# Kernel optimization log

Hardware: AMD Instinct MI355X
Metric: run time of the kernel (lower is better)

Reference implementation:

```python
import jax, jax.numpy as jnp
import numpy as np

T = 36  # num_frames


def box_cxcywh_to_xyxy(b):
    cx, cy, w, h = jnp.split(b, 4, axis=-1)
    return jnp.concatenate([cx - 0.5 * w, cy - 0.5 * h, cx + 0.5 * w, cy + 0.5 * h], axis=-1)


def multi_iou(b1, b2):
    # b1: [Q,1,T,4], b2: [1,N,T,4], xyxy -> iou [Q,N,T]
    lt = jnp.maximum(b1[..., :2], b2[..., :2])
    rb = jnp.minimum(b1[..., 2:], b2[..., 2:])
    wh = jnp.clip(rb - lt, 0.0)
    inter = wh[..., 0] * wh[..., 1]
    a1 = (b1[..., 2] - b1[..., 0]) * (b1[..., 3] - b1[..., 1])
    a2 = (b2[..., 2] - b2[..., 0]) * (b2[..., 3] - b2[..., 1])
    union = a1 + a2 - inter
    return inter / union


def setup_inputs() -> dict:
    key = jax.random.key(0)
    k1, k2, k3, k4, k5, k6 = jax.random.split(key, 6)
    Q, N, C = 2048, 128, 42
    return {
        "pred_logits": jax.random.normal(k1, (T * Q, C), dtype=jnp.float32),
        "pred_boxes": jax.random.uniform(k2, (T * Q, 4), dtype=jnp.float32),
        "tgt_labels": jax.random.randint(k3, (N * T,), 0, C - 1),
        "tgt_boxes": jax.random.uniform(k4, (N * T, 4), dtype=jnp.float32),
        "tgt_valid": jax.random.randint(k5, (N * T,), 0, 2, dtype=jnp.int32),
        "tgt_original_valid": jax.random.randint(k6, (N * T,), 0, 2, dtype=jnp.int32),
    }


def reference(pred_logits, pred_boxes, tgt_labels, tgt_boxes, tgt_valid, tgt_original_valid):
    # Cost-matrix computation of SoftMaxHungarianMatcher (cost_class=cost_bbox=cost_giou=1,
    # use_giou=False, use_l1_distance_sum=False). The scipy linear_sum_assignment step is
    # CPU-serial / non-tensor and excluded; output is the [Q,N] cost fed to it.
    C = pred_logits.shape[-1]
    Q = pred_logits.shape[0] // T
    N = tgt_labels.shape[0] // T
    num_classes = C - 1  # background index

    probs = jax.nn.softmax(pred_logits, axis=-1).reshape(T, Q, C).transpose(1, 0, 2)  # [Q,T,C]
    boxes = pred_boxes.reshape(T, Q, 4).transpose(1, 0, 2)                            # [Q,T,4]
    tboxes = tgt_boxes.reshape(N, T, 4)
    valid = tgt_valid.reshape(N, T).astype(probs.dtype)                               # [N,T]
    ovalid = tgt_original_valid.reshape(N, T)
    ids = jnp.where(ovalid == 0, num_classes, tgt_labels.reshape(N, T))               # [N,T]

    denom = valid.sum(-1)  # [N] (per-instance count of valid frames)

    # class cost: -mean_t p(q, t, ids[n,t]) over valid frames
    gathered = probs[:, jnp.arange(T)[None, :], ids]                                  # [Q,N,T]
    class_cost = -(gathered * valid).sum(-1) / denom                                  # [Q,N]

    # bbox L1 cost: mean over (valid frames, 4 coords)
    l1 = jnp.abs(boxes[:, None] - tboxes[None]).mean(-1)                              # [Q,N,T]
    bbox_cost = (l1 * valid).sum(-1) / denom                                          # [Q,N]

    # IoU cost: -mean_t iou over valid frames
    iou = multi_iou(box_cxcywh_to_xyxy(boxes)[:, None], box_cxcywh_to_xyxy(tboxes)[None])
    iou_cost = -(iou * valid).sum(-1) / denom                                         # [Q,N]

    return class_cost + bbox_cost + iou_cost
```

## Files before the change

kernel.cpp:

```cpp
#include <hip/hip_runtime.h>
#include <hip/hip_bf16.h>


constexpr int T = 36;
constexpr int Q = 2048;
constexpr int C = 42;
constexpr int N = 128;

__global__ __launch_bounds__(256) void softmax_transpose_kernel(
    const float* __restrict__ logits, __hip_bfloat16* __restrict__ P2) {
  constexpr int QB = 64;
  constexpr int LS = C + 1;

  __shared__ float tile[QB * LS];
  __shared__ float s_max[4 * QB];
  __shared__ float s_sum[4 * QB];
  __shared__ float s_rinv[QB];

  const int t = blockIdx.y;
  const int q0 = blockIdx.x * QB;
  const int tid = threadIdx.x;

  const float* src = logits + ((size_t)t * Q + q0) * C;
  for (int i = tid; i < QB * C; i += 256) {
    int r = i / C, c = i % C;
    tile[r * LS + c] = src[i];
  }
  __syncthreads();

  const int part = tid >> 6;
  const int row = tid & 63;
  const int c0 = (part < 2) ? part * 11 : 22 + (part - 2) * 10;
  const int c1 = (part < 2) ? c0 + 11 : c0 + 10;

  float m = -1e30f;
  for (int c = c0; c < c1; ++c) m = fmaxf(m, tile[row * LS + c]);
  s_max[part * QB + row] = m;
  __syncthreads();

  m = fmaxf(fmaxf(s_max[row], s_max[QB + row]),
            fmaxf(s_max[2 * QB + row], s_max[3 * QB + row]));
  float s = 0.f;
  for (int c = c0; c < c1; ++c) {
    float e = __expf(tile[row * LS + c] - m);
    tile[row * LS + c] = e;
    s += e;
  }
  s_sum[part * QB + row] = s;
  __syncthreads();

  if (part == 0) {
    float stot = s_sum[row] + s_sum[QB + row] + s_sum[2 * QB + row] +
                 s_sum[3 * QB + row];
    s_rinv[row] = 1.f / stot;
  }
  __syncthreads();

  for (int i = tid; i < QB * C / 2; i += 256) {
    int c = i >> 5;
    int r2 = i & 31;
    float v0 = tile[(2 * r2) * LS + c] * s_rinv[2 * r2];
    float v1 = tile[(2 * r2 + 1) * LS + c] * s_rinv[2 * r2 + 1];
    __hip_bfloat162 pk;
    pk.x = __float2bfloat16(v0);
    pk.y = __float2bfloat16(v1);
    *(__hip_bfloat162*)(P2 + (size_t)(t * C + c) * Q + q0 + 2 * r2) = pk;
  }
}

constexpr int NB = 8;

__global__ __launch_bounds__(512) void cost_kernel(
    const __hip_bfloat16* __restrict__ P2, const float* __restrict__ pred_boxes,
    const int* __restrict__ labels, const float* __restrict__ tboxes,
    const int* __restrict__ valid, const int* __restrict__ ovalid,
    float* __restrict__ out) {
  constexpr int RS = NB + 1;

  const int q0 = blockIdx.x * 64;
  const int n0 = blockIdx.y * NB;
  const int tid = threadIdx.x;
  const int lane = tid & 63;
  const int wave = tid >> 6;
  const int q = q0 + lane;

  __shared__ float4 s_tbA[NB * T];
  __shared__ float4 s_tbB[NB * T];
  __shared__ int s_pk[NB * T];
  __shared__ float s_rden[NB];
  __shared__ float s_red[8 * 64 * RS];

  for (int i = tid; i < NB * T; i += 512) {
    int n = n0 + i / T;
    int t = i % T;
    int g = n * T + t;
    int id = (ovalid[g] == 0) ? (C - 1) : labels[g];
    s_pk[i] = (valid[g] << 24) | (id * (Q * 2));
    float4 tb = ((const float4*)tboxes)[g];
    s_tbA[i] = tb;
    float4 B;
    B.x = fmaf(-0.5f, tb.z, tb.x);
    B.y = fmaf(-0.5f, tb.w, tb.y);
    B.z = fmaf(0.5f, tb.z, tb.x);
    B.w = fmaf(0.5f, tb.w, tb.y);
    s_tbB[i] = B;
  }
  if (tid < NB) {
    int n = n0 + tid;
    int s = 0;
    for (int t = 0; t < T; ++t) s += valid[n * T + t];
    s_rden[tid] = 1.f / (float)s;
  }
  __syncthreads();

  float acc[NB];
#pragma unroll
  for (int j = 0; j < NB; ++j) acc[j] = 0.f;

  const int t_begin = (wave * T) / 8;
  const int t_end = ((wave + 1) * T) / 8;

  for (int t = t_begin; t < t_end; ++t) {
    float4 pb = ((const float4*)pred_boxes)[t * Q + q];
    float px1 = fmaf(-0.5f, pb.z, pb.x);
    float py1 = fmaf(-0.5f, pb.w, pb.y);
    float px2 = fmaf(0.5f, pb.z, pb.x);
    float py2 = fmaf(0.5f, pb.w, pb.y);
    float area_p = pb.z * pb.w;
    const char* pcol = (const char*)(P2 + (size_t)t * C * Q + q);

#pragma unroll
    for (int j = 0; j < NB; ++j) {
      int pk = s_pk[j * T + t];
      if (pk & (1 << 24)) {
        float4 tb = s_tbA[j * T + t];
        float4 xy = s_tbB[j * T + t];
        float p = __bfloat162float(
            *(const __hip_bfloat16*)(pcol + (pk & 0xFFFFFF)));

        float s = fabsf(pb.x - tb.x) + fabsf(pb.y - tb.y) +
                  fabsf(pb.z - tb.z) + fabsf(pb.w - tb.w);
        float iw = fmaxf(fminf(px2, xy.z) - fmaxf(px1, xy.x), 0.f);
        float ih = fmaxf(fminf(py2, xy.w) - fmaxf(py1, xy.y), 0.f);
        float inter = iw * ih;
        float uni = fmaf(tb.z, tb.w, area_p) - inter;
        float r = __builtin_amdgcn_rcpf(uni);
        acc[j] = fmaf(0.25f, s, acc[j]) - p - inter * r;
      }
    }
  }

#pragma unroll
  for (int j = 0; j < NB; ++j) s_red[(wave * 64 + lane) * RS + j] = acc[j];
  __syncthreads();

  {
    int ql = tid >> 3;
    int j = tid & 7;
    float s = 0.f;
#pragma unroll
    for (int w = 0; w < 8; ++w) s += s_red[(w * 64 + ql) * RS + j];
    out[(size_t)(q0 + ql) * N + n0 + j] = s * s_rden[j];
  }
}

extern "C" void kernel_launch(void* const* d_in, const int* in_sizes, int n_in,
                              void* d_out, int out_size, void* d_ws, size_t ws_size,
                              hipStream_t stream) {
  const float* logits = (const float*)d_in[0];
  const float* pboxes = (const float*)d_in[1];
  const int* labels = (const int*)d_in[2];
  const float* tboxes = (const float*)d_in[3];
  const int* valid = (const int*)d_in[4];
  const int* ovalid = (const int*)d_in[5];
  float* out = (float*)d_out;

  __hip_bfloat16* P2 = (__hip_bfloat16*)d_ws;

  dim3 g1(Q / 64, T);
  softmax_transpose_kernel<<<g1, 256, 0, stream>>>(logits, P2);

  dim3 g2(Q / 64, N / NB);
  cost_kernel<<<g2, 512, 0, stream>>>(P2, pboxes, labels, tboxes, valid, ovalid, out);
}
```

Before: 86.27 us.

## Vectorize softmax without max-shift and repartition cost kernel per target

The softmax kernel now loads logits as float4, applies exp directly without subtracting the row max, and reduces row sums with wave shuffles instead of shared-memory staging. The cost kernel changes from 8 waves splitting frames with 8 targets per thread to 4 targets per block, each wave pair handling one target over half the frames. It also writes the output with float4 stores, and the grid doubles in the target dimension. Dropping the max subtraction risks overflow for large logits, and pred boxes are reloaded per target, which gives less reuse per thread.

```diff
diff --git a/kernel.cpp b/kernel.cpp
--- a/kernel.cpp
+++ b/kernel.cpp
@@ -10,57 +10,47 @@
 __global__ __launch_bounds__(256) void softmax_transpose_kernel(
     const float* __restrict__ logits, __hip_bfloat16* __restrict__ P2) {
   constexpr int QB = 64;
-  constexpr int LS = C + 1;
 
-  __shared__ float tile[QB * LS];
-  __shared__ float s_max[4 * QB];
-  __shared__ float s_sum[4 * QB];
+  __shared__ float tile[QB * C];
   __shared__ float s_rinv[QB];
 
   const int t = blockIdx.y;
   const int q0 = blockIdx.x * QB;
   const int tid = threadIdx.x;
 
-  const float* src = logits + ((size_t)t * Q + q0) * C;
-  for (int i = tid; i < QB * C; i += 256) {
-    int r = i / C, c = i % C;
-    tile[r * LS + c] = src[i];
+  {
+    const float4* src = (const float4*)(logits + ((size_t)t * Q + q0) * C);
+    float4* dst = (float4*)tile;
+    for (int i = tid; i < QB * C / 4; i += 256) {
+      float4 v = src[i];
+      float4 e;
+      e.x = __expf(v.x);
+      e.y = __expf(v.y);
+      e.z = __expf(v.z);
+      e.w = __expf(v.w);
+      dst[i] = e;
+    }
   }
   __syncthreads();
 
-  const int part = tid >> 6;
-  const int row = tid & 63;
-  const int c0 = (part < 2) ? part * 11 : 22 + (part - 2) * 10;
-  const int c1 = (part < 2) ? c0 + 11 : c0 + 10;
-
-  float m = -1e30f;
-  for (int c = c0; c < c1; ++c) m = fmaxf(m, tile[row * LS + c]);
-  s_max[part * QB + row] = m;
-  __syncthreads();
-
-  m = fmaxf(fmaxf(s_max[row], s_max[QB + row]),
-            fmaxf(s_max[2 * QB + row], s_max[3 * QB + row]));
-  float s = 0.f;
-  for (int c = c0; c < c1; ++c) {
-    float e = __expf(tile[row * LS + c] - m);
-    tile[row * LS + c] = e;
-    s += e;
-  }
-  s_sum[part * QB + row] = s;
-  __syncthreads();
-
-  if (part == 0) {
-    float stot = s_sum[row] + s_sum[QB + row] + s_sum[2 * QB + row] +
-                 s_sum[3 * QB + row];
-    s_rinv[row] = 1.f / stot;
+  {
+    const int row = tid >> 2;
+    const int part = tid & 3;
+    const int c0 = (part < 2) ? part * 11 : 22 + (part - 2) * 10;
+    const int c1 = (part < 2) ? c0 + 11 : c0 + 10;
+    float s = 0.f;
+    for (int c = c0; c < c1; ++c) s += tile[row * C + c];
+    s += __shfl_xor(s, 1);
+    s += __shfl_xor(s, 2);
+    if (part == 0) s_rinv[row] = __builtin_amdgcn_rcpf(s);
   }
   __syncthreads();
 
   for (int i = tid; i < QB * C / 2; i += 256) {
     int c = i >> 5;
     int r2 = i & 31;
-    float v0 = tile[(2 * r2) * LS + c] * s_rinv[2 * r2];
-    float v1 = tile[(2 * r2 + 1) * LS + c] * s_rinv[2 * r2 + 1];
+    float v0 = tile[(2 * r2) * C + c] * s_rinv[2 * r2];
+    float v1 = tile[(2 * r2 + 1) * C + c] * s_rinv[2 * r2 + 1];
     __hip_bfloat162 pk;
     pk.x = __float2bfloat16(v0);
     pk.y = __float2bfloat16(v1);
@@ -68,42 +58,33 @@
   }
 }
 
-constexpr int NB = 8;
-
 __global__ __launch_bounds__(512) void cost_kernel(
     const __hip_bfloat16* __restrict__ P2, const float* __restrict__ pred_boxes,
     const int* __restrict__ labels, const float* __restrict__ tboxes,
     const int* __restrict__ valid, const int* __restrict__ ovalid,
     float* __restrict__ out) {
+  constexpr int NB = 4;
   constexpr int RS = NB + 1;
 
   const int q0 = blockIdx.x * 64;
   const int n0 = blockIdx.y * NB;
   const int tid = threadIdx.x;
   const int lane = tid & 63;
-  const int wave = tid >> 6;
+  const int sub = (tid >> 6) & 3;
+  const int half = tid >> 8;
   const int q = q0 + lane;
 
-  __shared__ float4 s_tbA[NB * T];
-  __shared__ float4 s_tbB[NB * T];
-  __shared__ int s_pk[NB * T];
+  __shared__ float4 s_tb[NB * T];
+  __shared__ int s_idv[NB * T];
   __shared__ float s_rden[NB];
-  __shared__ float s_red[8 * 64 * RS];
+  __shared__ float s_res[2 * 64 * RS];
 
   for (int i = tid; i < NB * T; i += 512) {
     int n = n0 + i / T;
     int t = i % T;
     int g = n * T + t;
-    int id = (ovalid[g] == 0) ? (C - 1) : labels[g];
-    s_pk[i] = (valid[g] << 24) | (id * (Q * 2));
-    float4 tb = ((const float4*)tboxes)[g];
-    s_tbA[i] = tb;
-    float4 B;
-    B.x = fmaf(-0.5f, tb.z, tb.x);
-    B.y = fmaf(-0.5f, tb.w, tb.y);
-    B.z = fmaf(0.5f, tb.z, tb.x);
-    B.w = fmaf(0.5f, tb.w, tb.y);
-    s_tbB[i] = B;
+    s_idv[i] = ((ovalid[g] == 0) ? (C - 1) : labels[g]) | (valid[g] << 8);
+    s_tb[i] = ((const float4*)tboxes)[g];
   }
   if (tid < NB) {
     int n = n0 + tid;
@@ -113,54 +94,48 @@
   }
   __syncthreads();
 
-  float acc[NB];
-#pragma unroll
-  for (int j = 0; j < NB; ++j) acc[j] = 0.f;
-
-  const int t_begin = (wave * T) / 8;
-  const int t_end = ((wave + 1) * T) / 8;
+  float acc = 0.f;
+  const __hip_bfloat16* probs_base = P2 + q;
+  const int t_begin = half * (T / 2);
+  const int t_end = t_begin + (T / 2);
 
   for (int t = t_begin; t < t_end; ++t) {
-    float4 pb = ((const float4*)pred_boxes)[t * Q + q];
-    float px1 = fmaf(-0.5f, pb.z, pb.x);
-    float py1 = fmaf(-0.5f, pb.w, pb.y);
-    float px2 = fmaf(0.5f, pb.z, pb.x);
-    float py2 = fmaf(0.5f, pb.w, pb.y);
-    float area_p = pb.z * pb.w;
-    const char* pcol = (const char*)(P2 + (size_t)t * C * Q + q);
+    int pk = s_idv[sub * T + t];
+    if (pk & 0x100) {
+      float4 pb = ((const float4*)pred_boxes)[t * Q + q];
+      float4 tb = s_tb[sub * T + t];
+      int id = pk & 0xff;
+      float p = __bfloat162float(probs_base[(size_t)(t * C + id) * Q]);
 
-#pragma unroll
-    for (int j = 0; j < NB; ++j) {
-      int pk = s_pk[j * T + t];
-      if (pk & (1 << 24)) {
-        float4 tb = s_tbA[j * T + t];
-        float4 xy = s_tbB[j * T + t];
-        float p = __bfloat162float(
-            *(const __hip_bfloat16*)(pcol + (pk & 0xFFFFFF)));
-
-        float s = fabsf(pb.x - tb.x) + fabsf(pb.y - tb.y) +
-                  fabsf(pb.z - tb.z) + fabsf(pb.w - tb.w);
-        float iw = fmaxf(fminf(px2, xy.z) - fmaxf(px1, xy.x), 0.f);
-        float ih = fmaxf(fminf(py2, xy.w) - fmaxf(py1, xy.y), 0.f);
-        float inter = iw * ih;
-        float uni = fmaf(tb.z, tb.w, area_p) - inter;
-        float r = __builtin_amdgcn_rcpf(uni);
-        acc[j] = fmaf(0.25f, s, acc[j]) - p - inter * r;
-      }
+      float l1 = 0.25f * (fabsf(pb.x - tb.x) + fabsf(pb.y - tb.y) +
+                          fabsf(pb.z - tb.z) + fabsf(pb.w - tb.w));
+      float px1 = pb.x - 0.5f * pb.z, py1 = pb.y - 0.5f * pb.w;
+      float px2 = pb.x + 0.5f * pb.z, py2 = pb.y + 0.5f * pb.w;
+      float tx1 = tb.x - 0.5f * tb.z, ty1 = tb.y - 0.5f * tb.w;
+      float tx2 = tb.x + 0.5f * tb.z, ty2 = tb.y + 0.5f * tb.w;
+      float iw = fmaxf(fminf(px2, tx2) - fmaxf(px1, tx1), 0.f);
+      float ih = fmaxf(fminf(py2, ty2) - fmaxf(py1, ty1), 0.f);
+      float inter = iw * ih;
+      float uni = pb.z * pb.w + tb.z * tb.w - inter;
+      acc += l1 - p - inter * __builtin_amdgcn_rcpf(uni);
     }
   }
 
-#pragma unroll
-  for (int j = 0; j < NB; ++j) s_red[(wave * 64 + lane) * RS + j] = acc[j];
+  s_res[half * (64 * RS) + lane * RS + sub] = acc;
+  __syncthreads();
+  if (half == 0) {
+    float tot = (acc + s_res[64 * RS + lane * RS + sub]) * s_rden[sub];
+    s_res[lane * RS + sub] = tot;
+  }
   __syncthreads();
 
-  {
-    int ql = tid >> 3;
-    int j = tid & 7;
-    float s = 0.f;
-#pragma unroll
-    for (int w = 0; w < 8; ++w) s += s_red[(w * 64 + ql) * RS + j];
-    out[(size_t)(q0 + ql) * N + n0 + j] = s * s_rden[j];
+  if (tid < 64) {
+    float4 o;
+    o.x = s_res[tid * RS + 0];
+    o.y = s_res[tid * RS + 1];
+    o.z = s_res[tid * RS + 2];
+    o.w = s_res[tid * RS + 3];
+    *(float4*)(out + (size_t)(q0 + tid) * N + n0) = o;
   }
 }
 
@@ -180,6 +155,6 @@
   dim3 g1(Q / 64, T);
   softmax_transpose_kernel<<<g1, 256, 0, stream>>>(logits, P2);
 
-  dim3 g2(Q / 64, N / NB);
+  dim3 g2(Q / 64, N / 4);
   cost_kernel<<<g2, 512, 0, stream>>>(P2, pboxes, labels, tboxes, valid, ovalid, out);
 }
```

Result: faster. 81.51 us, median of 2 (-5.5%).
